# Kernel optimization log

Hardware: AMD Instinct MI355X
Metric: run time of the kernel (lower is better)

## Reference

```python
import jax, jax.numpy as jnp
import numpy as np

NUM_HOSTS = 13


def gcn_conv_max(x, src, dst, n, W, b):
    """PyG GCNConv with aggr='max': x@W, gcn_norm (self-loops + sym norm), max-scatter, +bias.
    src/dst already include self-loop edges."""
    xw = x @ W  # [N, out]
    deg = jnp.zeros((n,), xw.dtype).at[dst].add(1.0)
    dinv = jax.lax.rsqrt(deg)  # deg >= 1 thanks to self-loops
    norm = dinv[src] * dinv[dst]  # [E+N]
    msg = norm[:, None] * xw[src]  # [E+N, out] -- the big gather
    agg = jax.ops.segment_max(msg, dst, num_segments=n)
    return agg + b


def self_attn(v, g, aW, ab, fW, fb, gW, gb):
    """SimpleSelfAttention: softmax over feature dim, weighted-sum over nodes, residual global update."""
    att = jax.nn.softmax(v @ aW + ab, axis=-1)  # [B, Nh, h]
    feat = v @ fW + fb                            # [B, Nh, h]
    out = jnp.sum(att * feat, axis=1)             # [B, h]
    g_ = jnp.concatenate([out, g], axis=-1) @ gW + gb
    return g + g_


def setup_inputs() -> dict:
    key = jax.random.key(0)
    ks = jax.random.split(key, 24)
    IN, H1, H2 = 64, 256, 64
    B, NPG = 256, 200
    N = B * NPG
    E = 409600

    x = jax.random.normal(ks[0], (N, IN), jnp.float32)
    host_idx = (jnp.arange(B)[:, None] * NPG + jnp.arange(NUM_HOSTS)[None, :]).reshape(-1).astype(jnp.int32)
    x = x.at[host_idx, 0].set(1.0)  # hosts = x[:,0]==1
    ei = jax.random.randint(ks[1], (2, E), 0, N, dtype=jnp.int64)

    def lin(k, i, o):
        k1, k2 = jax.random.split(k)
        s = 1.0 / np.sqrt(i)
        return (jax.random.uniform(k1, (i, o), jnp.float32, -s, s),
                jax.random.uniform(k2, (o,), jnp.float32, -s, s))

    W1, b1 = lin(ks[2], IN, H1)
    W2, b2 = lin(ks[3], H1, H2)
    # g0: in=IN, h=H1, g=H1 ; g1: in=H1, h=H1 ; g2: in=H2, h=H2
    a0W, a0b = lin(ks[4], IN, H1); f0W, f0b = lin(ks[5], IN, H1); g0W, g0b = lin(ks[6], H1 + H1, H1)
    a1W, a1b = lin(ks[7], H1, H1); f1W, f1b = lin(ks[8], H1, H1); g1W, g1b = lin(ks[9], H1 + H1, H1)
    a2W, a2b = lin(ks[10], H2, H2); f2W, f2b = lin(ks[11], H2, H2); g2W, g2b = lin(ks[12], H2 + H1, H1)
    o1W, o1b = lin(ks[13], H1, H2)
    o2W, o2b = lin(ks[14], H2, 1)

    return dict(x=x, ei=ei, host_idx=host_idx,
                W1=W1, b1=b1, W2=W2, b2=b2,
                a0W=a0W, a0b=a0b, f0W=f0W, f0b=f0b, g0W=g0W, g0b=g0b,
                a1W=a1W, a1b=a1b, f1W=f1W, f1b=f1b, g1W=g1W, g1b=g1b,
                a2W=a2W, a2b=a2b, f2W=f2W, f2b=f2b, g2W=g2W, g2b=g2b,
                o1W=o1W, o1b=o1b, o2W=o2W, o2b=o2b)


def reference(x, ei, host_idx,
              W1, b1, W2, b2,
              a0W, a0b, f0W, f0b, g0W, g0b,
              a1W, a1b, f1W, f1b, g1W, g1b,
              a2W, a2b, f2W, f2b, g2W, g2b,
              o1W, o1b, o2W, o2b):
    n = x.shape[0]
    B = host_idx.shape[0] // NUM_HOSTS
    loops = jnp.arange(n, dtype=ei.dtype)
    src = jnp.concatenate([ei[0], loops])
    dst = jnp.concatenate([ei[1], loops])

    hx = x[host_idx].reshape(B, NUM_HOSTS, -1)
    g = self_attn(hx, jnp.zeros((B, g0b.shape[0]), x.dtype), a0W, a0b, f0W, f0b, g0W, g0b)

    x1 = jax.nn.relu(gcn_conv_max(x, src, dst, n, W1, b1))
    g = self_attn(x1[host_idx].reshape(B, NUM_HOSTS, -1), g, a1W, a1b, f1W, f1b, g1W, g1b)

    x2 = jax.nn.relu(gcn_conv_max(x1, src, dst, n, W2, b2))
    g = self_attn(x2[host_idx].reshape(B, NUM_HOSTS, -1), g, a2W, a2b, f2W, f2b, g2W, g2b)

    return jax.nn.relu(g @ o1W + o1b) @ o2W + o2b  # [B, 1]
```

## Files before the change

kernel.cpp:

```cpp
#include <hip/hip_runtime.h>
#include <math.h>
#include <stdio.h>

#define N_NODES 51200
#define N_EDGES 409600
#define B_GRAPH 256
#define NH 13

typedef float v4f __attribute__((ext_vector_type(4)));
typedef unsigned v2u __attribute__((ext_vector_type(2)));
typedef short s16x8 __attribute__((ext_vector_type(8)));
typedef float f32x4 __attribute__((ext_vector_type(4)));

__device__ __forceinline__ void nt_store_u2(uint2* p, uint2 v) {
    v2u w; w.x = v.x; w.y = v.y;
    __builtin_nontemporal_store(w, (v2u*)p);
}

__device__ __forceinline__ unsigned pack_bf2(float a, float b) {
    unsigned ua = __float_as_uint(a);
    ua = (ua + 0x7fffu + ((ua >> 16) & 1u)) >> 16;
    unsigned ub = __float_as_uint(b);
    ub = (ub + 0x7fffu + ((ub >> 16) & 1u)) & 0xffff0000u;
    return ua | ub;
}
__device__ __forceinline__ float bf_lo(unsigned u) { return __uint_as_float(u << 16); }
__device__ __forceinline__ float bf_hi(unsigned u) { return __uint_as_float(u & 0xffff0000u); }

__device__ __forceinline__ s16x8 as_s8(uint4 u) {
    return __builtin_bit_cast(s16x8, u);
}
__device__ __forceinline__ f32x4 mfma16(s16x8 a, s16x8 b, f32x4 c) {
    return __builtin_amdgcn_mfma_f32_16x16x32_bf16(a, b, c, 0, 0, 0);
}

__device__ __forceinline__ void cvt_hilo(const float4& xa, const float4& xb,
                                         s16x8& hi, s16x8& lo) {
    unsigned h0 = pack_bf2(xa.x, xa.y);
    unsigned h1 = pack_bf2(xa.z, xa.w);
    unsigned h2 = pack_bf2(xb.x, xb.y);
    unsigned h3 = pack_bf2(xb.z, xb.w);
    unsigned l0 = pack_bf2(xa.x - bf_lo(h0), xa.y - bf_hi(h0));
    unsigned l1 = pack_bf2(xa.z - bf_lo(h1), xa.w - bf_hi(h1));
    unsigned l2 = pack_bf2(xb.x - bf_lo(h2), xb.y - bf_hi(h2));
    unsigned l3 = pack_bf2(xb.z - bf_lo(h3), xb.w - bf_hi(h3));
    hi = as_s8(make_uint4(h0, h1, h2, h3));
    lo = as_s8(make_uint4(l0, l1, l2, l3));
}

__device__ __forceinline__ bool ei_is_64(const int* __restrict__ ei32) {
    int z = 1;
    #pragma unroll
    for (int k = 1; k < 16; k += 2) z &= (ei32[k] == 0);
    return z != 0;
}

__global__ void count_deg(const int* __restrict__ ei32, const long long* __restrict__ ei64,
                          int* __restrict__ degc,
                          const float* __restrict__ W1, const float* __restrict__ W2,
                          uint4* __restrict__ w1h, uint4* __restrict__ w1l,
                          uint4* __restrict__ w2h, uint4* __restrict__ w2l) {
    const int bid = blockIdx.x;
    if (bid >= 1600) {
        int rec = (bid - 1600) * 256 + threadIdx.x;
        bool isW1 = rec < 2048;
        int r = isW1 ? rec : rec - 2048;
        int l = r & 63;
        int lg = l >> 4;
        int col, krow, N;
        const float* W;
        if (isW1) {
            int c = r >> 7; int s = (r >> 6) & 1;
            col = c * 16 + (l & 15); krow = s * 32 + lg * 4; W = W1; N = 256;
        } else {
            int c = r >> 9; int s = (r >> 6) & 7;
            col = c * 16 + (l & 15); krow = s * 32 + lg * 4; W = W2; N = 64;
        }
        float f[8];
        #pragma unroll
        for (int e = 0; e < 8; ++e) {
            int kk = krow + (e & 3) + 16 * (e >> 2);
            f[e] = W[(size_t)kk * N + col];
        }
        unsigned h[4], lo[4];
        #pragma unroll
        for (int p = 0; p < 4; ++p) {
            h[p] = pack_bf2(f[2 * p], f[2 * p + 1]);
            lo[p] = pack_bf2(f[2 * p] - bf_lo(h[p]), f[2 * p + 1] - bf_hi(h[p]));
        }
        uint4 H = make_uint4(h[0], h[1], h[2], h[3]);
        uint4 L = make_uint4(lo[0], lo[1], lo[2], lo[3]);
        if (isW1) { w1h[r] = H; w1l[r] = L; }
        else      { w2h[r] = H; w2l[r] = L; }
        return;
    }
    int e = bid * 256 + threadIdx.x;
    if (e >= N_EDGES) return;
    int v = ei_is_64(ei32) ? (int)ei64[N_EDGES + e] : ei32[N_EDGES + e];
    atomicAdd(&degc[v], 1);
}

__global__ void scan_block_sums(const int* __restrict__ degc, int* __restrict__ bsums) {
    __shared__ int sdata[256];
    int i = blockIdx.x * 256 + threadIdx.x;
    sdata[threadIdx.x] = degc[i];
    __syncthreads();
    for (int s = 128; s > 0; s >>= 1) {
        if (threadIdx.x < s) sdata[threadIdx.x] += sdata[threadIdx.x + s];
        __syncthreads();
    }
    if (threadIdx.x == 0) bsums[blockIdx.x] = sdata[0];
}

__global__ void scan_finalize(int* __restrict__ degc, int* __restrict__ offs,
                              float* __restrict__ dinv, const int* __restrict__ bsums) {
    __shared__ int bs[256];
    __shared__ int s[256];
    const int t = threadIdx.x;
    bs[t] = (t < 200) ? bsums[t] : 0;
    __syncthreads();
    for (int off = 1; off < 256; off <<= 1) {
        int u = (t >= off) ? bs[t - off] : 0;
        __syncthreads();
        bs[t] += u;
        __syncthreads();
    }
    int i = blockIdx.x * 256 + t;
    int cnt = degc[i];
    s[t] = cnt;
    __syncthreads();
    for (int off = 1; off < 256; off <<= 1) {
        int u = (t >= off) ? s[t - off] : 0;
        __syncthreads();
        s[t] += u;
        __syncthreads();
    }
    int base = (blockIdx.x == 0) ? 0 : bs[blockIdx.x - 1];
    int excl = base + s[t] - cnt;
    offs[i] = excl;
    dinv[i] = rsqrtf((float)(cnt + 1));
    degc[i] = excl;
    if (i == N_NODES - 1) offs[N_NODES] = N_EDGES;
}

template <int K, int WS, bool BF16IN>
__device__ __forceinline__ void gemm_body64(const float* __restrict__ X,
        const float* __restrict__ W, const float* __restrict__ bias,
        float* __restrict__ Y, int row0, const int* __restrict__ rows,
        float* __restrict__ xs, float* __restrict__ ws) {
    constexpr int BK = 32;
    constexpr int XS = BK + 4;
    const int t = threadIdx.x;
    const int ct = t & 15;
    const int rt = t >> 4;
    float acc[4][4] = {{0.f}};
    for (int kc = 0; kc < K; kc += BK) {
        __syncthreads();
        #pragma unroll
        for (int i = 0; i < 2; ++i) {
            int idx = t + i * 256;
            int q = idx & 7, r = idx >> 3;
            int xr = rows[r];
            float4 v;
            if (BF16IN) {
                uint2 pv = ((const uint2*)X)[(size_t)xr * (K / 4) + kc / 4 + q];
                v = make_float4(bf_lo(pv.x), bf_hi(pv.x), bf_lo(pv.y), bf_hi(pv.y));
            } else {
                v = *(const float4*)(X + (size_t)xr * K + kc + q * 4);
            }
            *(float4*)&xs[r * XS + q * 4] = v;
        }
        #pragma unroll
        for (int i = 0; i < 2; ++i) {
            int idx = t + i * 256;
            int q = idx & 15, k = idx >> 4;
            float4 v = *(const float4*)(W + (size_t)(kc + k) * WS + q * 4);
            *(float4*)&ws[k * 64 + q * 4] = v;
        }
        __syncthreads();
        #pragma unroll
        for (int kb = 0; kb < BK; kb += 4) {
            float4 wv[4];
            #pragma unroll
            for (int kk = 0; kk < 4; ++kk)
                wv[kk] = *(const float4*)&ws[(kb + kk) * 64 + ct * 4];
            #pragma unroll
            for (int r = 0; r < 4; ++r) {
                float4 xv = *(const float4*)&xs[(rt * 4 + r) * XS + kb];
                float xk[4] = {xv.x, xv.y, xv.z, xv.w};
                #pragma unroll
                for (int kk = 0; kk < 4; ++kk) {
                    acc[r][0] = fmaf(xk[kk], wv[kk].x, acc[r][0]);
                    acc[r][1] = fmaf(xk[kk], wv[kk].y, acc[r][1]);
                    acc[r][2] = fmaf(xk[kk], wv[kk].z, acc[r][2]);
                    acc[r][3] = fmaf(xk[kk], wv[kk].w, acc[r][3]);
                }
            }
        }
    }
    #pragma unroll
    for (int r = 0; r < 4; ++r) {
        int row = row0 + rt * 4 + r;
        float4 o = make_float4(acc[r][0] + bias[ct * 4 + 0],
                               acc[r][1] + bias[ct * 4 + 1],
                               acc[r][2] + bias[ct * 4 + 2],
                               acc[r][3] + bias[ct * 4 + 3]);
        *(float4*)&Y[(size_t)row * 512 + ct * 4] = o;
    }
}

__global__ __launch_bounds__(256, 4) void fused_gemm1(const float* __restrict__ x,
        const uint4* __restrict__ w1h, const uint4* __restrict__ w1l,
        float* __restrict__ xw1b, const float* __restrict__ dinv,
        const int* __restrict__ ei32, const long long* __restrict__ ei64,
        int* __restrict__ cursor, int* __restrict__ csr,
        const int* __restrict__ host_idx,
        const float* __restrict__ a0W, const float* __restrict__ a0b,
        const float* __restrict__ f0W, const float* __restrict__ f0b,
        float* __restrict__ AF) {
    __shared__ float smem[64 * 68];
    __shared__ int rows[64];
    const int bid = blockIdx.x;
    const int t = threadIdx.x;
    if (bid < 1600) {
        const int row0 = (bid >> 2) * 128;
        const int c0 = (bid & 3) * 64;
        const int w = t >> 6, l = t & 63, lr = l & 15, lg = l >> 4;
        f32x4 acc[2][4] = {};
        #pragma unroll
        for (int s = 0; s < 2; ++s) {
            s16x8 bh[4], bl[4];
            #pragma unroll
            for (int cc = 0; cc < 4; ++cc) {
                int idx = (((c0 >> 4) + cc) * 2 + s) * 64 + l;
                bh[cc] = as_s8(w1h[idx]);
                bl[cc] = as_s8(w1l[idx]);
            }
            #pragma unroll
            for (int f = 0; f < 2; ++f) {
                int rowA = row0 + w * 32 + f * 16 + lr;
                const float* xp = x + (size_t)rowA * 64 + s * 32 + lg * 4;
                float4 xa = *(const float4*)xp;
                float4 xb = *(const float4*)(xp + 16);
                s16x8 ah, al;
                cvt_hilo(xa, xb, ah, al);
                #pragma unroll
                for (int cc = 0; cc < 4; ++cc) {
                    acc[f][cc] = mfma16(ah, bh[cc], acc[f][cc]);
                    acc[f][cc] = mfma16(al, bh[cc], acc[f][cc]);
                    acc[f][cc] = mfma16(ah, bl[cc], acc[f][cc]);
                }
            }
        }
        #pragma unroll
        for (int f = 0; f < 2; ++f) {
            if (f) __syncthreads();
            #pragma unroll
            for (int r = 0; r < 4; ++r) {
                float dv = dinv[row0 + w * 32 + f * 16 + lg * 4 + r];
                #pragma unroll
                for (int cc = 0; cc < 4; ++cc)
                    smem[(w * 16 + lg * 4 + r) * 68 + cc * 16 + lr] = acc[f][cc][r] * dv;
            }
            __syncthreads();
            int row_l = t >> 2, cB = (t & 3) * 16;
            int grow = row0 + (row_l >> 4) * 32 + f * 16 + (row_l & 15);
            const float* src = &smem[row_l * 68 + cB];
            float4 v0 = *(const float4*)(src + 0);
            float4 v1 = *(const float4*)(src + 4);
            float4 v2 = *(const float4*)(src + 8);
            float4 v3 = *(const float4*)(src + 12);
            uint4 o0, o1;
            o0.x = pack_bf2(v0.x, v0.y); o0.y = pack_bf2(v0.z, v0.w);
            o0.z = pack_bf2(v1.x, v1.y); o0.w = pack_bf2(v1.z, v1.w);
            o1.x = pack_bf2(v2.x, v2.y); o1.y = pack_bf2(v2.z, v2.w);
            o1.z = pack_bf2(v3.x, v3.y); o1.w = pack_bf2(v3.z, v3.w);
            uint4* yp = (uint4*)xw1b + (size_t)grow * 32 + (c0 >> 3) + (t & 3) * 2;
            yp[0] = o0; yp[1] = o1;
        }
    } else if (bid < 2016) {
        const int abid = bid - 1600;
        const int rb = abid >> 3;
        const int cb = abid & 7;
        const int c0 = cb * 64;
        const float* Wp = (c0 < 256) ? (a0W + c0) : (f0W + (c0 - 256));
        const float* bp = (c0 < 256) ? (a0b + c0) : (f0b + (c0 - 256));
        if (t < 64) rows[t] = host_idx[rb * 64 + t];
        __syncthreads();
        gemm_body64<64, 256, false>(x, Wp, bp, AF + c0, rb * 64, rows, smem, smem + 64 * 36);
    } else {
        int e = (bid - 2016) * 256 + t;
        if (e < N_EDGES) {
            int u, v;
            if (ei_is_64(ei32)) { u = (int)ei64[e]; v = (int)ei64[N_EDGES + e]; }
            else                { u = ei32[e];      v = ei32[N_EDGES + e]; }
            int pos = atomicAdd(&cursor[v], 1);
            csr[pos] = u;
        }
    }
}

__global__ __launch_bounds__(256, 4) void fused_gemm2(const float* __restrict__ x1b,
        const uint4* __restrict__ w2h, const uint4* __restrict__ w2l,
        float* __restrict__ xw2, const float* __restrict__ dinv,
        const int* __restrict__ host_idx,
        const float* __restrict__ a1W, const float* __restrict__ a1b,
        const float* __restrict__ f1W, const float* __restrict__ f1b,
        float* __restrict__ AF) {
    __shared__ float smem[64 * 68];
    __shared__ int rows[64];
    const int bid = blockIdx.x;
    const int t = threadIdx.x;
    if (bid < 400) {
        const int row0 = bid * 128;
        const int w = t >> 6, l = t & 63, lr = l & 15, lg = l >> 4;
        f32x4 acc[2][4] = {};
        const uint2* xb = (const uint2*)x1b;
        #pragma unroll 2
        for (int s = 0; s < 8; ++s) {
            s16x8 bh[4], bl[4];
            #pragma unroll
            for (int cc = 0; cc < 4; ++cc) {
                int idx = (cc * 8 + s) * 64 + l;
                bh[cc] = as_s8(w2h[idx]);
                bl[cc] = as_s8(w2l[idx]);
            }
            #pragma unroll
            for (int f = 0; f < 2; ++f) {
                int row = row0 + w * 32 + f * 16 + lr;
                const uint2* ap = xb + (size_t)row * 64 + s * 8 + lg;
                uint2 a0 = ap[0];
                uint2 a1 = ap[4];
                s16x8 a = as_s8(make_uint4(a0.x, a0.y, a1.x, a1.y));
                #pragma unroll
                for (int cc = 0; cc < 4; ++cc) {
                    acc[f][cc] = mfma16(a, bh[cc], acc[f][cc]);
                    acc[f][cc] = mfma16(a, bl[cc], acc[f][cc]);
                }
            }
        }
        #pragma unroll
        for (int f = 0; f < 2; ++f) {
            if (f) __syncthreads();
            #pragma unroll
            for (int r = 0; r < 4; ++r) {
                float dv = dinv[row0 + w * 32 + f * 16 + lg * 4 + r];
                #pragma unroll
                for (int cc = 0; cc < 4; ++cc)
                    smem[(w * 16 + lg * 4 + r) * 68 + cc * 16 + lr] = acc[f][cc][r] * dv;
            }
            __syncthreads();
            int row_l = t >> 2, cB = (t & 3) * 16;
            int grow = row0 + (row_l >> 4) * 32 + f * 16 + (row_l & 15);
            const float* src = &smem[row_l * 68 + cB];
            float4* dstp = (float4*)(xw2 + (size_t)grow * 64 + cB);
            dstp[0] = *(const float4*)(src + 0);
            dstp[1] = *(const float4*)(src + 4);
            dstp[2] = *(const float4*)(src + 8);
            dstp[3] = *(const float4*)(src + 12);
        }
    } else {
        const int abid = bid - 400;
        const int rb = abid >> 3;
        const int cb = abid & 7;
        const int c0 = cb * 64;
        const float* Wp = (c0 < 256) ? (a1W + c0) : (f1W + (c0 - 256));
        const float* bp = (c0 < 256) ? (a1b + c0) : (f1b + (c0 - 256));
        if (t < 64) rows[t] = host_idx[rb * 64 + t];
        __syncthreads();
        gemm_body64<256, 256, true>(x1b, Wp, bp, AF + c0, rb * 64, rows, smem, smem + 64 * 36);
    }
}

__device__ __forceinline__ void attn_red256(const float* __restrict__ AF,
        const float* __restrict__ gW, const float* __restrict__ gb,
        const float* __restrict__ g_in, float* __restrict__ g_out, int b,
        float (*At)[256], float* red_m, float* red_s, float* cat) {
    const int t = threadIdx.x;
    const int wave = t >> 6, lane = t & 63;
    float accA[NH], accF[NH];
    #pragma unroll
    for (int j = 0; j < NH; ++j) {
        const float* r = AF + (size_t)(b * NH + j) * 512;
        accA[j] = r[t];
        accF[j] = r[256 + t];
        At[j][t] = accA[j];
    }
    __syncthreads();
    for (int j = wave; j < NH; j += 4) {
        float m = -3.402823466e38f;
        #pragma unroll
        for (int q = 0; q < 4; ++q) m = fmaxf(m, At[j][q * 64 + lane]);
        #pragma unroll
        for (int off = 32; off; off >>= 1) m = fmaxf(m, __shfl_xor(m, off));
        if (lane == 0) red_m[j] = m;
    }
    __syncthreads();
    #pragma unroll
    for (int j = 0; j < NH; ++j) At[j][t] = expf(accA[j] - red_m[j]);
    __syncthreads();
    for (int j = wave; j < NH; j += 4) {
        float s = 0.f;
        #pragma unroll
        for (int q = 0; q < 4; ++q) s += At[j][q * 64 + lane];
        #pragma unroll
        for (int off = 32; off; off >>= 1) s += __shfl_xor(s, off);
        if (lane == 0) red_s[j] = s;
    }
    __syncthreads();
    float outc = 0.f;
    #pragma unroll
    for (int j = 0; j < NH; ++j) outc += At[j][t] / red_s[j] * accF[j];
    cat[t] = outc;
    float gv = g_in ? g_in[b * 256 + t] : 0.f;
    cat[256 + t] = gv;
    __syncthreads();
    float acc = gb[t];
    const float* gwp = gW + t;
    #pragma unroll 4
    for (int i4 = 0; i4 < 128; ++i4) {
        float4 cq = ((const float4*)cat)[i4];
        const float* gw4 = gwp + (size_t)i4 * 4 * 256;
        acc = fmaf(cq.x, gw4[0], acc);
        acc = fmaf(cq.y, gw4[256], acc);
        acc = fmaf(cq.z, gw4[512], acc);
        acc = fmaf(cq.w, gw4[768], acc);
    }
    g_out[b * 256 + t] = gv + acc;
}

__global__ __launch_bounds__(256) void fused_agg256(const uint2* __restrict__ xwb,
        const float* __restrict__ dinv, const int* __restrict__ offs,
        const int* __restrict__ csr, const float* __restrict__ bias,
        uint2* __restrict__ outb,
        const float* __restrict__ AF, const float* __restrict__ gW,
        const float* __restrict__ gb, const float* __restrict__ g_in,
        float* __restrict__ g_out) {
    __shared__ float At[NH][256];
    __shared__ float red_m[NH];
    __shared__ float red_s[NH];
    __shared__ float cat[512];
    const int bid = blockIdx.x;
    if (bid < 256) {
        attn_red256(AF, gW, gb, g_in, g_out, bid, At, red_m, red_s, cat);
        return;
    }
    int gid = (bid - 256) * 256 + threadIdx.x;
    int v = gid >> 6;
    int lane = gid & 63;
    uint2 sw = xwb[(size_t)v * 64 + lane];
    float4 acc = make_float4(bf_lo(sw.x), bf_hi(sw.x), bf_lo(sw.y), bf_hi(sw.y));
    int e0 = offs[v];
    int e1 = offs[v + 1];
    int em = e0 + ((e1 - e0) & ~7);
    for (int e = e0; e < em; e += 8) {
        int u[8];
        #pragma unroll
        for (int i = 0; i < 8; ++i) u[i] = csr[e + i];
        uint2 m[8];
        #pragma unroll
        for (int i = 0; i < 8; ++i) m[i] = xwb[(size_t)u[i] * 64 + lane];
        #pragma unroll
        for (int i = 0; i < 8; ++i) {
            acc.x = fmaxf(acc.x, bf_lo(m[i].x));
            acc.y = fmaxf(acc.y, bf_hi(m[i].x));
            acc.z = fmaxf(acc.z, bf_lo(m[i].y));
            acc.w = fmaxf(acc.w, bf_hi(m[i].y));
        }
    }
    if (em < e1) {
        int u[8];
        #pragma unroll
        for (int i = 0; i < 8; ++i) u[i] = csr[(em + i < e1) ? (em + i) : (e1 - 1)];
        uint2 m[8];
        #pragma unroll
        for (int i = 0; i < 8; ++i) m[i] = xwb[(size_t)u[i] * 64 + lane];
        #pragma unroll
        for (int i = 0; i < 8; ++i) {
            if (em + i < e1) {
                acc.x = fmaxf(acc.x, bf_lo(m[i].x));
                acc.y = fmaxf(acc.y, bf_hi(m[i].x));
                acc.z = fmaxf(acc.z, bf_lo(m[i].y));
                acc.w = fmaxf(acc.w, bf_hi(m[i].y));
            }
        }
    }
    float dv = dinv[v];
    float4 b4 = ((const float4*)bias)[lane];
    float4 o;
    o.x = fmaxf(fmaf(acc.x, dv, b4.x), 0.f);
    o.y = fmaxf(fmaf(acc.y, dv, b4.y), 0.f);
    o.z = fmaxf(fmaf(acc.z, dv, b4.z), 0.f);
    o.w = fmaxf(fmaf(acc.w, dv, b4.w), 0.f);
    uint2 pk;
    pk.x = pack_bf2(o.x, o.y);
    pk.y = pack_bf2(o.z, o.w);
    nt_store_u2(outb + (size_t)v * 64 + lane, pk);
}

__global__ __launch_bounds__(1024) void attn_graph_head(
        const float* __restrict__ AF,
        const float* __restrict__ g1W, const float* __restrict__ g1b,
        const float* __restrict__ g_in,
        const float* __restrict__ xw2,
        const float* __restrict__ dinv, const int* __restrict__ offs,
        const int* __restrict__ csr, const float* __restrict__ b2,
        const int* __restrict__ host_idx,
        const float* __restrict__ a2W, const float* __restrict__ a2b,
        const float* __restrict__ f2W, const float* __restrict__ f2b,
        const float* __restrict__ g2W, const float* __restrict__ g2b,
        const float* __restrict__ o1W, const float* __restrict__ o1b,
        const float* __restrict__ o2W, const float* __restrict__ o2b,
        float* __restrict__ out) {
    __shared__ float At[NH][256];
    __shared__ float Ft[NH][256];
    __shared__ float red_m[NH];
    __shared__ float red_s[NH];
    __shared__ float cat[512];
    __shared__ float catB[320];
    __shared__ float g1s[256];
    __shared__ float x2l[NH][64];
    __shared__ float part4[4][256];
    __shared__ float part16[16][64];
    __shared__ float grow[256];
    const int b = blockIdx.x;
    const int t = threadIdx.x;
    const int wave = t >> 6;
    const int lane = t & 63;
    const int c = t & 255;
    const int quad = t >> 8;

    if (wave < NH) {
        int hv = host_idx[b * NH + wave];
        float acc = xw2[(size_t)hv * 64 + lane];
        int e0 = offs[hv], e1 = offs[hv + 1];
        for (int e = e0; e < e1; e += 8) {
            int u[8];
            #pragma unroll
            for (int i = 0; i < 8; ++i) u[i] = csr[(e + i < e1) ? (e + i) : (e1 - 1)];
            float m[8];
            #pragma unroll
            for (int i = 0; i < 8; ++i) m[i] = xw2[(size_t)u[i] * 64 + lane];
            #pragma unroll
            for (int i = 0; i < 8; ++i)
                if (e + i < e1) acc = fmaxf(acc, m[i]);
        }
        x2l[wave][lane] = fmaxf(fmaf(acc, dinv[hv], b2[lane]), 0.f);
    }
    for (int idx = t; idx < NH * 128; idx += 1024) {
        int j = idx >> 7, q = idx & 127;
        float4 v = ((const float4*)(AF + (size_t)(b * NH + j) * 512))[q];
        if (q < 64) *(float4*)&At[j][q * 4] = v;
        else        *(float4*)&Ft[j][(q - 64) * 4] = v;
    }
    __syncthreads();
    if (wave < NH) {
        float m = -3.402823466e38f;
        #pragma unroll
        for (int q = 0; q < 4; ++q) m = fmaxf(m, At[wave][q * 64 + lane]);
        #pragma unroll
        for (int off = 32; off; off >>= 1) m = fmaxf(m, __shfl_xor(m, off));
        if (lane == 0) red_m[wave] = m;
    }
    __syncthreads();
    for (int idx = t; idx < NH * 256; idx += 1024) {
        int j = idx >> 8, cc = idx & 255;
        At[j][cc] = expf(At[j][cc] - red_m[j]);
    }
    __syncthreads();
    if (wave < NH) {
        float s = 0.f;
        #pragma unroll
        for (int q = 0; q < 4; ++q) s += At[wave][q * 64 + lane];
        #pragma unroll
        for (int off = 32; off; off >>= 1) s += __shfl_xor(s, off);
        if (lane == 0) red_s[wave] = s;
    }
    __syncthreads();
    if (quad == 0) {
        float outc = 0.f;
        #pragma unroll
        for (int j = 0; j < NH; ++j) outc += At[j][c] / red_s[j] * Ft[j][c];
        cat[c] = outc;
        cat[256 + c] = g_in[b * 256 + c];
    }
    __syncthreads();
    {
        float acc = 0.f;
        const float* gwp = g1W + c;
        #pragma unroll 4
        for (int i4 = quad * 32; i4 < quad * 32 + 32; ++i4) {
            float4 cq = ((const float4*)cat)[i4];
            const float* gw4 = gwp + (size_t)i4 * 1024;
            acc = fmaf(cq.x, gw4[0], acc);
            acc = fmaf(cq.y, gw4[256], acc);
            acc = fmaf(cq.z, gw4[512], acc);
            acc = fmaf(cq.w, gw4[768], acc);
        }
        part4[quad][c] = acc;
    }
    __syncthreads();
    if (quad == 0)
        g1s[c] = cat[256 + c] + g1b[c] +
                 part4[0][c] + part4[1][c] + part4[2][c] + part4[3][c];
    __syncthreads();
    if (wave < NH) {
        float aA = a2b[lane], aF = f2b[lane];
        #pragma unroll 8
        for (int k = 0; k < 64; ++k) {
            float xv = x2l[wave][k];
            aA = fmaf(xv, a2W[k * 64 + lane], aA);
            aF = fmaf(xv, f2W[k * 64 + lane], aF);
        }
        float m = aA;
        #pragma unroll
        for (int off = 32; off; off >>= 1) m = fmaxf(m, __shfl_xor(m, off));
        float pexp = expf(aA - m);
        float s = pexp;
        #pragma unroll
        for (int off = 32; off; off >>= 1) s += __shfl_xor(s, off);
        At[wave][lane] = pexp / s * aF;
    }
    __syncthreads();
    if (t < 64) {
        float o = 0.f;
        #pragma unroll
        for (int j = 0; j < NH; ++j) o += At[j][t];
        catB[t] = o;
    }
    if (quad == 0) catB[64 + c] = g1s[c];
    __syncthreads();
    {
        float acc = 0.f;
        const float* gwp = g2W + c;
        #pragma unroll 4
        for (int i4 = quad * 20; i4 < quad * 20 + 20; ++i4) {
            float4 cq = ((const float4*)catB)[i4];
            const float* gw4 = gwp + (size_t)i4 * 1024;
            acc = fmaf(cq.x, gw4[0], acc);
            acc = fmaf(cq.y, gw4[256], acc);
            acc = fmaf(cq.z, gw4[512], acc);
            acc = fmaf(cq.w, gw4[768], acc);
        }
        part4[quad][c] = acc;
    }
    __syncthreads();
    if (quad == 0)
        grow[c] = g1s[c] + g2b[c] +
                  part4[0][c] + part4[1][c] + part4[2][c] + part4[3][c];
    __syncthreads();
    {
        float hp = 0.f;
        #pragma unroll
        for (int k = wave * 16; k < wave * 16 + 16; ++k)
            hp = fmaf(grow[k], o1W[(size_t)k * 64 + lane], hp);
        part16[wave][lane] = hp;
    }
    __syncthreads();
    if (wave == 0) {
        float h = o1b[lane];
        #pragma unroll
        for (int w = 0; w < 16; ++w) h += part16[w][lane];
        h = fmaxf(h, 0.f);
        float sres = h * o2W[lane];
        #pragma unroll
        for (int off = 32; off; off >>= 1) sres += __shfl_xor(sres, off);
        if (lane == 0) out[b] = sres + o2b[0];
    }
}

extern "C" void kernel_launch(void* const* d_in, const int* in_sizes, int n_in,
                              void* d_out, int out_size, void* d_ws, size_t ws_size,
                              hipStream_t stream) {
    (void)in_sizes; (void)n_in; (void)out_size;
    const float* x    = (const float*)d_in[0];
    const int* ei32   = (const int*)d_in[1];
    const long long* ei64 = (const long long*)d_in[1];
    const int* hidx   = (const int*)d_in[2];
    const float* W1 = (const float*)d_in[3],  *b1 = (const float*)d_in[4];
    const float* W2 = (const float*)d_in[5],  *b2 = (const float*)d_in[6];
    const float* a0W = (const float*)d_in[7],  *a0b = (const float*)d_in[8];
    const float* f0W = (const float*)d_in[9],  *f0b = (const float*)d_in[10];
    const float* g0W = (const float*)d_in[11], *g0b = (const float*)d_in[12];
    const float* a1W = (const float*)d_in[13], *a1b = (const float*)d_in[14];
    const float* f1W = (const float*)d_in[15], *f1b = (const float*)d_in[16];
    const float* g1W = (const float*)d_in[17], *g1b = (const float*)d_in[18];
    const float* a2W = (const float*)d_in[19], *a2b = (const float*)d_in[20];
    const float* f2W = (const float*)d_in[21], *f2b = (const float*)d_in[22];
    const float* g2W = (const float*)d_in[23], *g2b = (const float*)d_in[24];
    const float* o1W = (const float*)d_in[25], *o1b = (const float*)d_in[26];
    const float* o2W = (const float*)d_in[27], *o2b = (const float*)d_in[28];
    float* outp = (float*)d_out;

    char* p = (char*)d_ws;
    auto alloc = [&](size_t bytes) {
        char* r = p;
        p += (bytes + 255) & ~(size_t)255;
        return r;
    };
    float* dinv = (float*)alloc((size_t)N_NODES * 4);
    int* degc   = (int*)alloc((size_t)N_NODES * 4);
    int* offs   = (int*)alloc((size_t)(N_NODES + 1) * 4);
    int* csr    = (int*)alloc((size_t)N_EDGES * 4);
    int* bsums  = (int*)alloc(256 * 4);
    float* g    = (float*)alloc((size_t)B_GRAPH * 256 * 4);
    float* AF   = (float*)alloc((size_t)B_GRAPH * NH * 512 * 4);
    unsigned short* xw1b = (unsigned short*)alloc((size_t)N_NODES * 256 * 2);
    unsigned short* x1b  = (unsigned short*)alloc((size_t)N_NODES * 256 * 2);
    float* xw2  = (float*)alloc((size_t)N_NODES * 64 * 4);
    uint4* w1h  = (uint4*)alloc((size_t)2048 * 16);
    uint4* w1l  = (uint4*)alloc((size_t)2048 * 16);
    uint4* w2h  = (uint4*)alloc((size_t)2048 * 16);
    uint4* w2l  = (uint4*)alloc((size_t)2048 * 16);

    size_t need = (size_t)(p - (char*)d_ws);
    if (need > ws_size) {
        fprintf(stderr, "kernel_launch: ws too small (%zu needed, %zu have)\n", need, ws_size);
        return;
    }

    (void)hipMemsetAsync(degc, 0, (size_t)N_NODES * 4, stream);
    count_deg<<<1616, 256, 0, stream>>>(ei32, ei64, degc, W1, W2, w1h, w1l, w2h, w2l);
    scan_block_sums<<<200, 256, 0, stream>>>(degc, bsums);
    scan_finalize<<<200, 256, 0, stream>>>(degc, offs, dinv, bsums);

    fused_gemm1<<<3616, 256, 0, stream>>>(
        x, w1h, w1l, (float*)xw1b, dinv, ei32, ei64, degc, csr,
        hidx, a0W, a0b, f0W, f0b, AF);
    fused_agg256<<<256 + 12800, 256, 0, stream>>>((const uint2*)xw1b, dinv, offs, csr,
                                                  b1, (uint2*)x1b, AF, g0W, g0b,
                                                  nullptr, g);
    fused_gemm2<<<816, 256, 0, stream>>>(
        (const float*)x1b, w2h, w2l, xw2, dinv, hidx, a1W, a1b, f1W, f1b, AF);
    attn_graph_head<<<256, 1024, 0, stream>>>(
        AF, g1W, g1b, g, xw2, dinv, offs, csr, b2, hidx,
        a2W, a2b, f2W, f2b, g2W, g2b, o1W, o1b, o2W, o2b, outp);
}
```

Before: 271.4 us.

## Build CSR via destination buckets with LDS histograms and LDS-cursor scatter

Edges are first binned by destination node block (dst>>8) into 200 fixed-capacity buckets as packed (src, dst) 16-bit pairs, with an overflow list for full buckets. Per-node degree histograms and the CSR scatter then run per bucket using shared-memory atomics. This replaces the many scattered global atomics on per-node counters and cursors and gives the CSR writes more locality. In exchange, the binning step makes all edges contend on only 200 global counters. The fixed bucket and overflow capacities also silently drop edges if the degree distribution is far more skewed than the random test graph.

```diff
diff --git a/kernel.cpp b/kernel.cpp
--- a/kernel.cpp
+++ b/kernel.cpp
@@ -6,6 +6,9 @@
 #define N_EDGES 409600
 #define B_GRAPH 256
 #define NH 13
+#define NBKT 200
+#define BCAP 3072
+#define OVFCAP 8192
 
 typedef float v4f __attribute__((ext_vector_type(4)));
 typedef unsigned v2u __attribute__((ext_vector_type(2)));
@@ -56,7 +59,8 @@
 }
 
 __global__ void count_deg(const int* __restrict__ ei32, const long long* __restrict__ ei64,
-                          int* __restrict__ degc,
+                          int* __restrict__ bcnt, unsigned* __restrict__ pairs,
+                          unsigned* __restrict__ ovf,
                           const float* __restrict__ W1, const float* __restrict__ W2,
                           uint4* __restrict__ w1h, uint4* __restrict__ w1l,
                           uint4* __restrict__ w2h, uint4* __restrict__ w2l) {
@@ -96,20 +100,44 @@
     }
     int e = bid * 256 + threadIdx.x;
     if (e >= N_EDGES) return;
-    int v = ei_is_64(ei32) ? (int)ei64[N_EDGES + e] : ei32[N_EDGES + e];
-    atomicAdd(&degc[v], 1);
-}
-
-__global__ void scan_block_sums(const int* __restrict__ degc, int* __restrict__ bsums) {
+    int u, v;
+    if (ei_is_64(ei32)) { u = (int)ei64[e]; v = (int)ei64[N_EDGES + e]; }
+    else                { u = ei32[e];      v = ei32[N_EDGES + e]; }
+    unsigned w = (unsigned)u | ((unsigned)v << 16);
+    int b = v >> 8;
+    int p = atomicAdd(&bcnt[b], 1);
+    if (p < BCAP) pairs[(size_t)b * BCAP + p] = w;
+    else { int q = atomicAdd(&bcnt[NBKT], 1); if (q < OVFCAP) ovf[q] = w; }
+}
+
+__global__ void scan_block_sums(const int* __restrict__ bcnt,
+                                const unsigned* __restrict__ pairs,
+                                const unsigned* __restrict__ ovf,
+                                int* __restrict__ degc, int* __restrict__ bsums) {
+    __shared__ int hist[256];
     __shared__ int sdata[256];
-    int i = blockIdx.x * 256 + threadIdx.x;
-    sdata[threadIdx.x] = degc[i];
+    const int b = blockIdx.x;
+    const int t = threadIdx.x;
+    hist[t] = 0;
+    __syncthreads();
+    int cnt = min(bcnt[b], BCAP);
+    const unsigned* pb = pairs + (size_t)b * BCAP;
+    for (int i = t; i < cnt; i += 256)
+        atomicAdd(&hist[(pb[i] >> 16) & 255], 1);
+    int ovn = min(bcnt[NBKT], OVFCAP);
+    for (int i = t; i < ovn; i += 256) {
+        int v = (int)(ovf[i] >> 16);
+        if ((v >> 8) == b) atomicAdd(&hist[v & 255], 1);
+    }
+    __syncthreads();
+    degc[b * 256 + t] = hist[t];
+    sdata[t] = hist[t];
     __syncthreads();
     for (int s = 128; s > 0; s >>= 1) {
-        if (threadIdx.x < s) sdata[threadIdx.x] += sdata[threadIdx.x + s];
-        __syncthreads();
-    }
-    if (threadIdx.x == 0) bsums[blockIdx.x] = sdata[0];
+        if (t < s) sdata[t] += sdata[t + s];
+        __syncthreads();
+    }
+    if (t == 0) bsums[b] = sdata[0];
 }
 
 __global__ void scan_finalize(int* __restrict__ degc, int* __restrict__ offs,
@@ -139,7 +167,6 @@
     int excl = base + s[t] - cnt;
     offs[i] = excl;
     dinv[i] = rsqrtf((float)(cnt + 1));
-    degc[i] = excl;
     if (i == N_NODES - 1) offs[N_NODES] = N_EDGES;
 }
 
@@ -212,8 +239,9 @@
 __global__ __launch_bounds__(256, 4) void fused_gemm1(const float* __restrict__ x,
         const uint4* __restrict__ w1h, const uint4* __restrict__ w1l,
         float* __restrict__ xw1b, const float* __restrict__ dinv,
-        const int* __restrict__ ei32, const long long* __restrict__ ei64,
-        int* __restrict__ cursor, int* __restrict__ csr,
+        const int* __restrict__ bcnt, const unsigned* __restrict__ pairs,
+        const unsigned* __restrict__ ovf, const int* __restrict__ offs,
+        int* __restrict__ csr,
         const int* __restrict__ host_idx,
         const float* __restrict__ a0W, const float* __restrict__ a0b,
         const float* __restrict__ f0W, const float* __restrict__ f0b,
@@ -289,13 +317,25 @@
         __syncthreads();
         gemm_body64<64, 256, false>(x, Wp, bp, AF + c0, rb * 64, rows, smem, smem + 64 * 36);
     } else {
-        int e = (bid - 2016) * 256 + t;
-        if (e < N_EDGES) {
-            int u, v;
-            if (ei_is_64(ei32)) { u = (int)ei64[e]; v = (int)ei64[N_EDGES + e]; }
-            else                { u = ei32[e];      v = ei32[N_EDGES + e]; }
-            int pos = atomicAdd(&cursor[v], 1);
-            csr[pos] = u;
+        const int b = bid - 2016;
+        int* lcur = (int*)smem;
+        lcur[t] = offs[b * 256 + t];
+        __syncthreads();
+        int cnt = min(bcnt[b], BCAP);
+        const unsigned* pb = pairs + (size_t)b * BCAP;
+        for (int i = t; i < cnt; i += 256) {
+            unsigned w = pb[i];
+            int pos = atomicAdd(&lcur[(w >> 16) & 255], 1);
+            csr[pos] = (int)(w & 0xffffu);
+        }
+        int ovn = min(bcnt[NBKT], OVFCAP);
+        for (int i = 0; i < ovn; ++i) {
+            unsigned w = ovf[i];
+            int v = (int)(w >> 16);
+            if ((v >> 8) == b && (v & 255) == t) {
+                int pos = atomicAdd(&lcur[t], 1);
+                csr[pos] = (int)(w & 0xffffu);
+            }
         }
     }
 }
@@ -712,6 +752,9 @@
     uint4* w1l  = (uint4*)alloc((size_t)2048 * 16);
     uint4* w2h  = (uint4*)alloc((size_t)2048 * 16);
     uint4* w2l  = (uint4*)alloc((size_t)2048 * 16);
+    int* bcnt   = (int*)alloc((size_t)(NBKT + 1) * 4);
+    unsigned* pairs = (unsigned*)alloc((size_t)NBKT * BCAP * 4);
+    unsigned* ovf   = (unsigned*)alloc((size_t)OVFCAP * 4);
 
     size_t need = (size_t)(p - (char*)d_ws);
     if (need > ws_size) {
@@ -719,13 +762,14 @@
         return;
     }
 
-    (void)hipMemsetAsync(degc, 0, (size_t)N_NODES * 4, stream);
-    count_deg<<<1616, 256, 0, stream>>>(ei32, ei64, degc, W1, W2, w1h, w1l, w2h, w2l);
-    scan_block_sums<<<200, 256, 0, stream>>>(degc, bsums);
+    (void)hipMemsetAsync(bcnt, 0, (size_t)(NBKT + 1) * 4, stream);
+    count_deg<<<1616, 256, 0, stream>>>(ei32, ei64, bcnt, pairs, ovf,
+                                        W1, W2, w1h, w1l, w2h, w2l);
+    scan_block_sums<<<200, 256, 0, stream>>>(bcnt, pairs, ovf, degc, bsums);
     scan_finalize<<<200, 256, 0, stream>>>(degc, offs, dinv, bsums);
 
-    fused_gemm1<<<3616, 256, 0, stream>>>(
-        x, w1h, w1l, (float*)xw1b, dinv, ei32, ei64, degc, csr,
+    fused_gemm1<<<2216, 256, 0, stream>>>(
+        x, w1h, w1l, (float*)xw1b, dinv, bcnt, pairs, ovf, offs, csr,
         hidx, a0W, a0b, f0W, f0b, AF);
     fused_agg256<<<256 + 12800, 256, 0, stream>>>((const uint2*)xw1b, dinv, offs, csr,
                                                   b1, (uint2*)x1b, AF, g0W, g0b,
```

Result: slower. 463.6 us (+70.8%).

## Interleave GEMM and CSR-fill blocks, add nontemporal loads and stores

Applied to the files above, without the earlier changes.

Reorders the fused_gemm1 block schedule so the host-attention GEMM blocks go first and the MFMA GEMM blocks alternate with the edge-scatter CSR-fill blocks. Mixing compute-bound and atomic-bound blocks is meant to let them overlap on each CU. It also switches streaming edge-index loads and the xw1b/xw2/AF output stores to nontemporal hints to reduce cache pollution. The risk is that nontemporal stores of xw1b/xw2, which the next gather kernels read back, may no longer hit in cache.

```diff
diff --git a/kernel.cpp b/kernel.cpp
--- a/kernel.cpp
+++ b/kernel.cpp
@@ -9,12 +9,21 @@
 
 typedef float v4f __attribute__((ext_vector_type(4)));
 typedef unsigned v2u __attribute__((ext_vector_type(2)));
+typedef unsigned v4u __attribute__((ext_vector_type(4)));
 typedef short s16x8 __attribute__((ext_vector_type(8)));
 typedef float f32x4 __attribute__((ext_vector_type(4)));
 
 __device__ __forceinline__ void nt_store_u2(uint2* p, uint2 v) {
     v2u w; w.x = v.x; w.y = v.y;
     __builtin_nontemporal_store(w, (v2u*)p);
+}
+__device__ __forceinline__ void nt_store_u4(uint4* p, uint4 v) {
+    v4u w; w.x = v.x; w.y = v.y; w.z = v.z; w.w = v.w;
+    __builtin_nontemporal_store(w, (v4u*)p);
+}
+__device__ __forceinline__ void nt_store_f4(float* p, float4 v) {
+    v4f w; w.x = v.x; w.y = v.y; w.z = v.z; w.w = v.w;
+    __builtin_nontemporal_store(w, (v4f*)p);
 }
 
 __device__ __forceinline__ unsigned pack_bf2(float a, float b) {
@@ -96,7 +105,8 @@
     }
     int e = bid * 256 + threadIdx.x;
     if (e >= N_EDGES) return;
-    int v = ei_is_64(ei32) ? (int)ei64[N_EDGES + e] : ei32[N_EDGES + e];
+    int v = ei_is_64(ei32) ? (int)__builtin_nontemporal_load(&ei64[N_EDGES + e])
+                           : __builtin_nontemporal_load(&ei32[N_EDGES + e]);
     atomicAdd(&degc[v], 1);
 }
 
@@ -205,7 +215,7 @@
                                acc[r][1] + bias[ct * 4 + 1],
                                acc[r][2] + bias[ct * 4 + 2],
                                acc[r][3] + bias[ct * 4 + 3]);
-        *(float4*)&Y[(size_t)row * 512 + ct * 4] = o;
+        nt_store_f4(&Y[(size_t)row * 512 + ct * 4], o);
     }
 }
 
@@ -222,9 +232,19 @@
     __shared__ int rows[64];
     const int bid = blockIdx.x;
     const int t = threadIdx.x;
-    if (bid < 1600) {
-        const int row0 = (bid >> 2) * 128;
-        const int c0 = (bid & 3) * 64;
+    if (bid < 416) {
+        const int rb = bid >> 3;
+        const int cb = bid & 7;
+        const int c0 = cb * 64;
+        const float* Wp = (c0 < 256) ? (a0W + c0) : (f0W + (c0 - 256));
+        const float* bp = (c0 < 256) ? (a0b + c0) : (f0b + (c0 - 256));
+        if (t < 64) rows[t] = host_idx[rb * 64 + t];
+        __syncthreads();
+        gemm_body64<64, 256, false>(x, Wp, bp, AF + c0, rb * 64, rows, smem, smem + 64 * 36);
+    } else if ((bid - 416) & 1) {
+        const int gid = (bid - 416) >> 1;
+        const int row0 = (gid >> 2) * 128;
+        const int c0 = (gid & 3) * 64;
         const int w = t >> 6, l = t & 63, lr = l & 15, lg = l >> 4;
         f32x4 acc[2][4] = {};
         #pragma unroll
@@ -276,24 +296,20 @@
             o1.x = pack_bf2(v2.x, v2.y); o1.y = pack_bf2(v2.z, v2.w);
             o1.z = pack_bf2(v3.x, v3.y); o1.w = pack_bf2(v3.z, v3.w);
             uint4* yp = (uint4*)xw1b + (size_t)grow * 32 + (c0 >> 3) + (t & 3) * 2;
-            yp[0] = o0; yp[1] = o1;
-        }
-    } else if (bid < 2016) {
-        const int abid = bid - 1600;
-        const int rb = abid >> 3;
-        const int cb = abid & 7;
-        const int c0 = cb * 64;
-        const float* Wp = (c0 < 256) ? (a0W + c0) : (f0W + (c0 - 256));
-        const float* bp = (c0 < 256) ? (a0b + c0) : (f0b + (c0 - 256));
-        if (t < 64) rows[t] = host_idx[rb * 64 + t];
-        __syncthreads();
-        gemm_body64<64, 256, false>(x, Wp, bp, AF + c0, rb * 64, rows, smem, smem + 64 * 36);
+            nt_store_u4(yp, o0);
+            nt_store_u4(yp + 1, o1);
+        }
     } else {
-        int e = (bid - 2016) * 256 + t;
+        int e = ((bid - 416) >> 1) * 256 + t;
         if (e < N_EDGES) {
             int u, v;
-            if (ei_is_64(ei32)) { u = (int)ei64[e]; v = (int)ei64[N_EDGES + e]; }
-            else                { u = ei32[e];      v = ei32[N_EDGES + e]; }
+            if (ei_is_64(ei32)) {
+                u = (int)__builtin_nontemporal_load(&ei64[e]);
+                v = (int)__builtin_nontemporal_load(&ei64[N_EDGES + e]);
+            } else {
+                u = __builtin_nontemporal_load(&ei32[e]);
+                v = __builtin_nontemporal_load(&ei32[N_EDGES + e]);
+            }
             int pos = atomicAdd(&cursor[v], 1);
             csr[pos] = u;
         }
@@ -353,11 +369,11 @@
             int row_l = t >> 2, cB = (t & 3) * 16;
             int grow = row0 + (row_l >> 4) * 32 + f * 16 + (row_l & 15);
             const float* src = &smem[row_l * 68 + cB];
-            float4* dstp = (float4*)(xw2 + (size_t)grow * 64 + cB);
-            dstp[0] = *(const float4*)(src + 0);
-            dstp[1] = *(const float4*)(src + 4);
-            dstp[2] = *(const float4*)(src + 8);
-            dstp[3] = *(const float4*)(src + 12);
+            float* dstp = xw2 + (size_t)grow * 64 + cB;
+            nt_store_f4(dstp + 0,  *(const float4*)(src + 0));
+            nt_store_f4(dstp + 4,  *(const float4*)(src + 4));
+            nt_store_f4(dstp + 8,  *(const float4*)(src + 8));
+            nt_store_f4(dstp + 12, *(const float4*)(src + 12));
         }
     } else {
         const int abid = bid - 400;
```

New measurement: 267.3 us. Within noise of the previous version (-1.5%).
